# Optimization experiments

Hardware: AMD Instinct MI355X
Metric: run time of the kernel (lower is better)

## Reference

```python
import jax, jax.numpy as jnp
import numpy as np

PATCH = 16
FMAP = 14  # 224 // 16, feature-map / mask resolution
BLUR_K = np.array([[1., 2., 1.], [2., 4., 2.], [1., 2., 1.]], dtype=np.float32) / 16.0  # pascal(3), normalized


def _conv(x, w, stride, pad):
    return jax.lax.conv_general_dilated(
        x, w, (stride, stride), [(pad, pad), (pad, pad)],
        dimension_numbers=("NCHW", "OIHW", "NCHW"))


def _max_blur_pool(x):
    # MaxBlurPool2D(kernel_size=3, stride=2, max_pool_size=2, ceil_mode=False):
    x = jax.lax.reduce_window(x, -jnp.inf, jax.lax.max,
                              (1, 1, 2, 2), (1, 1, 1, 1), "VALID")
    C = x.shape[1]
    kw = jnp.broadcast_to(jnp.asarray(BLUR_K, x.dtype), (C, 1, 3, 3))
    return jax.lax.conv_general_dilated(
        x, kw, (2, 2), [(1, 1), (1, 1)],
        dimension_numbers=("NCHW", "OIHW", "NCHW"), feature_group_count=C)


def _up(m, hw):
    # upsample [B,1,FMAP,FMAP] mask to spatial size hw via repeat_interleave
    f = hw // FMAP
    return jnp.repeat(jnp.repeat(m, f, axis=2), f, axis=3)


def reference(x, masks, w1, w2):
    B = x.shape[0]
    m = masks.reshape(B, 1, FMAP, FMAP).astype(x.dtype)  # fmap-level active mask
    x = x * _up(m, x.shape[2])                 # _apply_masks: zero masked 16x16 patches
    x = _conv(x, w1, 2, 3)                     # B,64,112,112
    x = jax.nn.relu(x * _up(m, x.shape[2]))    # SparK-style sparse conv: re-mask output
    x = _max_blur_pool(x)                      # B,64,56,56
    x = _conv(x, w2, 2, 3)                     # B,768,28,28
    x = jax.nn.relu(x * _up(m, x.shape[2]))    # re-mask output of second sparse conv
    x = _max_blur_pool(x)                      # B,768,14,14
    B_, C, H, W = x.shape
    return x.reshape(B_, C, H * W).transpose(0, 2, 1)  # b (h w) c -> [B,196,768]


def setup_inputs() -> dict:
    key = jax.random.key(0)
    k1, k2, k3, k4 = jax.random.split(key, 4)
    x = jax.random.normal(k1, (64, 3, 224, 224), jnp.float32)
    masks = jax.random.randint(k2, (64, 196), 0, 2).astype(bool)
    # kaiming_normal fan_in scaling as in init_weight
    w1 = jax.random.normal(k3, (64, 3, 7, 7), jnp.float32) * np.float32(np.sqrt(2.0 / (3 * 49)))
    w2 = jax.random.normal(k4, (768, 64, 7, 7), jnp.float32) * np.float32(np.sqrt(2.0 / (64 * 49)))
    return {"x": x, "masks": masks, "w1": w1, "w2": w2}
```

## Files before the change

### kernel.cpp

```cpp
#include <hip/hip_runtime.h>
#include <stdint.h>

typedef __attribute__((ext_vector_type(8))) short short8;
typedef __attribute__((ext_vector_type(4))) float f32x4;

#define DEVFN static __device__ __forceinline__

DEVFN float bf2f(uint16_t u) { union { uint32_t i; float f; } v; v.i = ((uint32_t)u) << 16; return v.f; }
DEVFN uint16_t f2bf(float f) {
  union { float f; uint32_t i; } v; v.f = f;
  uint32_t u = v.i;
  u += 0x7fffu + ((u >> 16) & 1u);
  return (uint16_t)(u >> 16);
}
DEVFN int imin(int a, int b) { return a < b ? a : b; }

DEVFN void gl_lds16(const void* g, void* l) {
  __builtin_amdgcn_global_load_lds(
      (__attribute__((address_space(1))) void*)(void*)g,
      (__attribute__((address_space(3))) void*)l, 16, 0, 0);
}

DEVFN f32x4 mfma16(short8 a, short8 b, f32x4 c) {
  return __builtin_amdgcn_mfma_f32_16x16x32_bf16(a, b, c, 0, 0, 0);
}

static constexpr size_t OFF_XP   = 0;
static constexpr size_t OFF_W1T  = 27557888;
static constexpr size_t OFF_W2T  = 27586560;
static constexpr size_t OFF_Y1   = 32403456;
static constexpr size_t OFF_P1   = 135163904;
static constexpr size_t OFF_Y2   = 166653952;
static constexpr size_t OFF_LIST = 243724288;
static constexpr size_t OFF_CNT  = 243774464;
static constexpr size_t WS_NEED  = 243774664;

__global__ __launch_bounds__(256) void k_count(const int* __restrict__ masks, int* __restrict__ cnts) {
  int b = blockIdx.x;
  int gid = b * 256 + threadIdx.x;
  unsigned long long m = __ballot(masks[gid] != 0);
  __shared__ int wsum[4];
  if ((threadIdx.x & 63) == 0) wsum[threadIdx.x >> 6] = __popcll(m);
  __syncthreads();
  if (threadIdx.x == 0) cnts[b] = wsum[0] + wsum[1] + wsum[2] + wsum[3];
}

__global__ __launch_bounds__(256) void k_emit(const int* __restrict__ masks, const int* __restrict__ cnts,
                                              int* __restrict__ list, int* __restrict__ total) {
  int b = blockIdx.x;
  int gid = b * 256 + threadIdx.x;
  int lane = threadIdx.x & 63, wave = threadIdx.x >> 6;
  int base = 0;
  for (int i = 0; i < b; ++i) base += cnts[i];
  bool f = masks[gid] != 0;
  unsigned long long m = __ballot(f);
  __shared__ int wcnt[4];
  if (lane == 0) wcnt[wave] = __popcll(m);
  __syncthreads();
  int woff = 0;
  for (int i = 0; i < wave; ++i) woff += wcnt[i];
  if (f) list[base + woff + __popcll(m & ((1ull << lane) - 1ull))] = gid;
  if (b == 48 && threadIdx.x == 0)
    *total = base + wcnt[0] + wcnt[1] + wcnt[2] + wcnt[3];
}

__global__ __launch_bounds__(256) void k_prep(const float* __restrict__ x, const int* __restrict__ masks,
                                              uint16_t* __restrict__ xp) {
  int gid = blockIdx.x * 256 + threadIdx.x;
  int b = gid / 53824;
  int rc = gid - b * 53824;
  int r2 = rc / 232;
  int c2 = rc - r2 * 232;
  int r = r2 - 3, c = c2 - 3;
  uint16_t o0 = 0, o1 = 0, o2 = 0;
  if ((unsigned)r < 224u && (unsigned)c < 224u) {
    if (masks[b * 196 + (r >> 4) * 14 + (c >> 4)]) {
      const float* px = x + (((size_t)b * 3) * 224 + r) * 224 + c;
      o0 = f2bf(px[0]);
      o1 = f2bf(px[50176]);
      o2 = f2bf(px[100352]);
    }
  }
  ushort4 o; o.x = o0; o.y = o1; o.z = o2; o.w = 0;
  *(ushort4*)(xp + (size_t)gid * 4) = o;
}

__global__ __launch_bounds__(256) void k_wt(const float* __restrict__ w1, const float* __restrict__ w2,
                                            uint16_t* __restrict__ w1t, uint16_t* __restrict__ w2t) {
  int gid = blockIdx.x * 256 + threadIdx.x;
  if (gid < 14336) {
    int kh = gid / 2048; int r = gid - kh * 2048;
    int oc = r >> 5, slot = r & 31;
    int kw = slot >> 2, ic = slot & 3;
    float v = 0.f;
    if (kw < 7 && ic < 3) v = w1[((oc * 3 + ic) * 7 + kh) * 7 + kw];
    w1t[gid] = f2bf(v);
  } else {
    int g2 = gid - 14336;
    int khw = g2 / 49152; int r = g2 - khw * 49152;
    int oc = r >> 6, ic = r & 63;
    int kh = khw / 7, kw = khw - kh * 7;
    w2t[g2] = f2bf(w2[((oc * 64 + ic) * 7 + kh) * 7 + kw]);
  }
}

__global__ __launch_bounds__(256, 3) void k_conv1(const uint16_t* __restrict__ xp, const uint16_t* __restrict__ w1t,
                                                  const int* __restrict__ list, const int* __restrict__ count,
                                                  uint16_t* __restrict__ y1) {
  __shared__ uint16_t sB[7 * 64 * 32];
  __shared__ int sc[2];

  int cnt = *count;
  int blk = blockIdx.x;
  if (blk * 2 >= cnt) return;
  int tid = threadIdx.x, lane = tid & 63, wave = tid >> 6;
  int csw = (lane & 3) ^ ((lane >> 2) & 3);

  {
    const char* wg = (const char*)w1t;
    char* wl = (char*)sB;
#pragma unroll
    for (int t = 0; t < 7; ++t) {
      int ldsoff = t * 4096 + wave * 1024;
      int goff = t * 4096 + (wave * 16 + (lane >> 2)) * 64 + csw * 16;
      gl_lds16(wg + goff, wl + ldsoff);
    }
  }
  if (tid < 2) sc[tid] = list[imin(blk * 2 + tid, cnt - 1)];
  __syncthreads();

  int wm = wave * 32, mrow = lane & 15, kg = lane >> 4;

  const uint16_t* baseA[2];
#pragma unroll
  for (int i = 0; i < 2; ++i) {
    int row = wm + 16 * i + mrow;
    int cell = sc[row >> 6];
    int b = cell / 196, cc = cell - b * 196;
    int ci = cc / 14, cj = cc - ci * 14;
    int p = row & 63;
    int oh = ci * 8 + (p >> 3), ow = cj * 8 + (p & 7);
    baseA[i] = xp + (((size_t)(b * 232 + 2 * oh)) * 232 + 2 * ow) * 4 + kg * 8;
  }
  int ksw = (kg ^ (mrow & 3)) * 8;

  f32x4 acc[2][4];
#pragma unroll
  for (int i = 0; i < 2; ++i)
#pragma unroll
    for (int j = 0; j < 4; ++j) acc[i][j] = f32x4{0.f, 0.f, 0.f, 0.f};

#pragma unroll
  for (int kh = 0; kh < 7; ++kh) {
    short8 a0 = *(const short8*)(baseA[0] + kh * 928);
    short8 a1 = *(const short8*)(baseA[1] + kh * 928);
    const uint16_t* Bk = sB + kh * 2048;
#pragma unroll
    for (int j = 0; j < 4; ++j) {
      short8 bj = *(const short8*)(Bk + (16 * j + mrow) * 32 + ksw);
      acc[0][j] = mfma16(a0, bj, acc[0][j]);
      acc[1][j] = mfma16(a1, bj, acc[1][j]);
    }
  }

#pragma unroll
  for (int i = 0; i < 2; ++i) {
    int rbase = wm + 16 * i;
    int cellidx = blk * 2 + (rbase >> 6);
    if (cellidx >= cnt) continue;
    int cell = sc[rbase >> 6];
    int b = cell / 196, cc = cell - b * 196;
    int ci = cc / 14, cj = cc - ci * 14;
#pragma unroll
    for (int j = 0; j < 4; ++j) {
      int oc = 16 * j + mrow;
#pragma unroll
      for (int r = 0; r < 4; ++r) {
        int row = rbase + kg * 4 + r;
        int p = row & 63;
        int oh = ci * 8 + (p >> 3), ow = cj * 8 + (p & 7);
        float v = acc[i][j][r];
        v = v > 0.f ? v : 0.f;
        y1[(((size_t)(b * 112 + oh)) * 112 + ow) * 64 + oc] = f2bf(v);
      }
    }
  }
}

__global__ __launch_bounds__(256) void k_pool1(const uint16_t* __restrict__ y1, const int* __restrict__ masks,
                                               uint16_t* __restrict__ p1) {
  __shared__ uint16_t sY[18 * 18 * 64];
  int b = blockIdx.y;
  int tile = blockIdx.x;
  int tr = tile >> 3, tc = tile & 7;
  int pr0 = tr * 8, pc0 = tc * 8;
  int R0 = 2 * pr0 - 7, C0 = 2 * pc0 - 7;
  int tid = threadIdx.x;
  const int* mb = masks + b * 196;

  for (int idx = tid; idx < 2592; idx += 256) {
    int pix = idx >> 3, ch = idx & 7;
    int pr = pix / 18, pc = pix - pr * 18;
    int r = R0 + pr, c = C0 + pc;
    short8 v = {0, 0, 0, 0, 0, 0, 0, 0};
    if ((unsigned)r < 112u && (unsigned)c < 112u && mb[(r >> 3) * 14 + (c >> 3)])
      v = *(const short8*)(y1 + (((size_t)(b * 112 + r)) * 112 + c) * 64 + ch * 8);
    *(short8*)(sY + ((size_t)(pr * 18 + pc)) * 64 + ch * 8) = v;
  }
  __syncthreads();

  for (int it = tid; it < 512; it += 256) {
    int opix = it >> 3, ch = it & 7;
    int lr = opix >> 3, lc = opix & 7;
    int pr = pr0 + lr, pc = pc0 + lc;
    if (pr >= 62 || pc >= 62) continue;
    int oh = pr - 3, ow = pc - 3;
    float acc[8] = {0.f, 0.f, 0.f, 0.f, 0.f, 0.f, 0.f, 0.f};
    if ((unsigned)oh < 56u && (unsigned)ow < 56u) {
      float hm_prev[3][8];
#pragma unroll
      for (int dd = 0; dd < 4; ++dd) {
        float yv[4][8];
        const uint16_t* src = sY + ((size_t)((2 * lr + dd) * 18 + 2 * lc)) * 64 + ch * 8;
#pragma unroll
        for (int e = 0; e < 4; ++e) {
          short8 t8 = *(const short8*)(src + e * 64);
#pragma unroll
          for (int k = 0; k < 8; ++k) yv[e][k] = bf2f((uint16_t)t8[k]);
        }
        float hm[3][8];
#pragma unroll
        for (int e = 0; e < 3; ++e) {
          int qc = 2 * ow - 1 + e;
          float cv = ((unsigned)qc <= 110u) ? 1.f : 0.f;
#pragma unroll
          for (int k = 0; k < 8; ++k) hm[e][k] = cv * fmaxf(yv[e][k], yv[e + 1][k]);
        }
        if (dd > 0) {
          int d = dd - 1;
          int qr = 2 * oh - 1 + d;
          if ((unsigned)qr <= 110u) {
            float wd = (d == 1) ? 2.f : 1.f;
#pragma unroll
            for (int e = 0; e < 3; ++e) {
              float w = wd * ((e == 1) ? 2.f : 1.f);
#pragma unroll
              for (int k = 0; k < 8; ++k) acc[k] += w * fmaxf(hm_prev[e][k], hm[e][k]);
            }
          }
        }
#pragma unroll
        for (int e = 0; e < 3; ++e)
#pragma unroll
          for (int k = 0; k < 8; ++k) hm_prev[e][k] = hm[e][k];
      }
#pragma unroll
      for (int k = 0; k < 8; ++k) acc[k] *= (1.f / 16.f);
    }
    short8 o;
#pragma unroll
    for (int k = 0; k < 8; ++k) o[k] = (short)f2bf(acc[k]);
    *(short8*)(p1 + (((size_t)(b * 62 + pr)) * 62 + pc) * 64 + ch * 8) = o;
  }
}

__global__ __launch_bounds__(512, 4) void k_conv2(const uint16_t* __restrict__ p1, const uint16_t* __restrict__ w2t,
                                                  const int* __restrict__ list, const int* __restrict__ count,
                                                  uint16_t* __restrict__ y2) {
  __shared__ uint16_t sA[256 * 64];
  __shared__ uint16_t sBt[128 * 64];

  int cnt = *count;
  int gx = blockIdx.x;
  int xcd = gx & 7, s = gx >> 3;
  int y = s % 6, mtl = s / 6;
  int mt = xcd + 8 * mtl;
  if (mt * 64 >= cnt) return;
  int ocb = y * 128;
  int tid = threadIdx.x, lane = tid & 63, wave = tid >> 6;
  int csw = (lane & 7) ^ ((lane >> 3) & 7);

  int* scs = (int*)sA;
  if (tid < 64) scs[tid] = list[imin(mt * 64 + tid, cnt - 1)];
  __syncthreads();
  int qm = wave & 3, qn = wave >> 2;
  int mrow = lane & 15, kg = lane >> 4;
  int cellA[4], cellE[4];
#pragma unroll
  for (int t = 0; t < 4; ++t) cellA[t] = scs[wave * 8 + t * 2 + (lane >> 5)];
#pragma unroll
  for (int i = 0; i < 4; ++i) cellE[i] = scs[qm * 16 + 4 * i + kg];
  __syncthreads();

  const char* gA[4];
#pragma unroll
  for (int t = 0; t < 4; ++t) {
    int r = wave * 32 + t * 8 + (lane >> 3);
    int cell = cellA[t];
    int b = cell / 196, cc = cell - b * 196;
    int ci = cc / 14, cj = cc - ci * 14;
    int p = r & 3;
    int oh = 2 * ci + (p >> 1), ow = 2 * cj + (p & 1);
    gA[t] = (const char*)p1 + (((size_t)(b * 62 + 2 * oh)) * 62 + 2 * ow) * 128 + csw * 16;
  }
  const char* gB[2];
#pragma unroll
  for (int t = 0; t < 2; ++t) {
    int oc = ocb + wave * 16 + t * 8 + (lane >> 3);
    gB[t] = (const char*)w2t + (size_t)oc * 128 + csw * 16;
  }

  f32x4 acc[4][4];
#pragma unroll
  for (int i = 0; i < 4; ++i)
#pragma unroll
    for (int j = 0; j < 4; ++j) acc[i][j] = f32x4{0.f, 0.f, 0.f, 0.f};

  int sw = mrow & 7;
  int kh = 0, kw = 0;

#pragma unroll 1
  for (int it = 0; it < 49; ++it) {
    size_t offA = (size_t)(kh * 62 + kw) * 128;
    size_t offB = (size_t)it * 98304;
    char* la = (char*)sA + (wave * 32) * 128;
    char* lb = (char*)sBt + (wave * 16) * 128;
#pragma unroll
    for (int t = 0; t < 4; ++t) gl_lds16(gA[t] + offA, la + t * 1024);
#pragma unroll
    for (int t = 0; t < 2; ++t) gl_lds16(gB[t] + offB, lb + t * 1024);
    __syncthreads();
#pragma unroll
    for (int ks = 0; ks < 2; ++ks) {
      int koff = ((ks * 4 + kg) ^ sw) * 8;
      short8 a[4], bb[4];
#pragma unroll
      for (int i = 0; i < 4; ++i)
        a[i] = *(const short8*)(sA + (qm * 64 + 16 * i + mrow) * 64 + koff);
#pragma unroll
      for (int j = 0; j < 4; ++j)
        bb[j] = *(const short8*)(sBt + (qn * 64 + 16 * j + mrow) * 64 + koff);
#pragma unroll
      for (int i = 0; i < 4; ++i)
#pragma unroll
        for (int j = 0; j < 4; ++j)
          acc[i][j] = mfma16(a[i], bb[j], acc[i][j]);
    }
    __syncthreads();
    if (++kw == 7) { kw = 0; ++kh; }
  }

#pragma unroll
  for (int i = 0; i < 4; ++i) {
    int cellslot = qm * 16 + 4 * i + kg;
    int cellidx = mt * 64 + cellslot;
    if (cellidx >= cnt) continue;
    int cell = cellE[i];
    int b = cell / 196, cc = cell - b * 196;
    int ci = cc / 14, cj = cc - ci * 14;
#pragma unroll
    for (int j = 0; j < 4; ++j) {
      int oc = ocb + qn * 64 + 16 * j + mrow;
#pragma unroll
      for (int r = 0; r < 4; ++r) {
        int oh = 2 * ci + (r >> 1), ow = 2 * cj + (r & 1);
        float v = acc[i][j][r];
        v = v > 0.f ? v : 0.f;
        y2[(((size_t)(b * 784)) + oh * 28 + ow) * 768 + oc] = f2bf(v);
      }
    }
  }
}

__global__ __launch_bounds__(256) void k_pool2(const uint16_t* __restrict__ y2, const int* __restrict__ masks,
                                               float* __restrict__ out) {
  __shared__ uint16_t sY[4 * 28 * 128];
  int chunk = blockIdx.x, pi = blockIdx.y, b = blockIdx.z;
  int ch0 = chunk * 128;
  int tid = threadIdx.x;
  const int* mb = masks + b * 196;

  for (int idx = tid; idx < 1792; idx += 256) {
    int rc = idx >> 4;
    int sub = idx & 15;
    int k = rc / 28, c = rc - k * 28;
    int r = 2 * pi - 1 + k;
    short8 v = {0, 0, 0, 0, 0, 0, 0, 0};
    if ((unsigned)r < 28u && mb[(r >> 1) * 14 + (c >> 1)])
      v = *(const short8*)(y2 + (((size_t)(b * 784)) + r * 28 + c) * 768 + ch0 + sub * 8);
    *(short8*)(sY + ((size_t)(k * 28 + c)) * 128 + sub * 8) = v;
  }
  __syncthreads();

  for (int idx = tid; idx < 1792; idx += 256) {
    int pj = idx >> 7, ch = idx & 127;
    float v[4][4];
#pragma unroll
    for (int e = 0; e < 4; ++e) {
      int col = 2 * pj - 1 + e;
      bool cv = (unsigned)col < 28u;
#pragma unroll
      for (int k = 0; k < 4; ++k)
        v[k][e] = cv ? bf2f(sY[((size_t)(k * 28 + col)) * 128 + ch]) : 0.f;
    }
    float acc = 0.f;
#pragma unroll
    for (int d = 0; d < 3; ++d) {
      int q = 2 * pi - 1 + d;
      float gd = ((unsigned)q <= 26u) ? ((d == 1) ? 2.f : 1.f) : 0.f;
      float s = 0.f;
#pragma unroll
      for (int e = 0; e < 3; ++e) {
        int q2 = 2 * pj - 1 + e;
        float ge = ((unsigned)q2 <= 26u) ? ((e == 1) ? 2.f : 1.f) : 0.f;
        float m = fmaxf(fmaxf(v[d][e], v[d + 1][e]), fmaxf(v[d][e + 1], v[d + 1][e + 1]));
        s += ge * m;
      }
      acc += gd * s;
    }
    out[(((size_t)(b * 196)) + pi * 14 + pj) * 768 + ch0 + ch] = acc * (1.f / 16.f);
  }
}

extern "C" void kernel_launch(void* const* d_in, const int* in_sizes, int n_in,
                              void* d_out, int out_size, void* d_ws, size_t ws_size,
                              hipStream_t stream) {
  const float* x     = (const float*)d_in[0];
  const int*   masks = (const int*)d_in[1];
  const float* w1    = (const float*)d_in[2];
  const float* w2    = (const float*)d_in[3];

  char* ws = (char*)d_ws;
  if (ws_size < WS_NEED) return;

  uint16_t* xp  = (uint16_t*)(ws + OFF_XP);
  uint16_t* w1t = (uint16_t*)(ws + OFF_W1T);
  uint16_t* w2t = (uint16_t*)(ws + OFF_W2T);
  uint16_t* y1  = (uint16_t*)(ws + OFF_Y1);
  uint16_t* p1  = (uint16_t*)(ws + OFF_P1);
  uint16_t* y2  = (uint16_t*)(ws + OFF_Y2);
  int* list     = (int*)(ws + OFF_LIST);
  int* cnts     = (int*)(ws + OFF_CNT);
  int* total    = cnts + 49;

  k_count<<<49, 256, 0, stream>>>(masks, cnts);
  k_emit<<<49, 256, 0, stream>>>(masks, cnts, list, total);
  k_prep<<<13456, 256, 0, stream>>>(x, masks, xp);
  k_wt<<<9464, 256, 0, stream>>>(w1, w2, w1t, w2t);
  k_conv1<<<6272, 256, 0, stream>>>(xp, w1t, list, total, y1);
  k_pool1<<<dim3(64, 64), 256, 0, stream>>>(y1, masks, p1);
  k_conv2<<<1200, 512, 0, stream>>>(p1, w2t, list, total, y2);
  k_pool2<<<dim3(6, 14, 64), 256, 0, stream>>>(y2, masks, (float*)d_out);
}
```

Baseline: 395.3 us.

## Fuse conv1 with max-blur-pool per active cell and tile the w2 transpose

Conv1 and the first MaxBlurPool are merged into one kernel. Each active mask cell computes a 14x14 conv1 output region with halo into LDS, then writes its pooled 56x56-level outputs straight to p1. This drops the y1 round trip through global memory and the separate pool launch. In exchange the halo conv work is recomputed per cell, a memset of p1 is added, and the w2 weight transpose is rewritten to coalesce through LDS. Halo outputs that belong to active neighbour cells are skipped, so each p1 position is written only once.

```diff
diff --git a/kernel.cpp b/kernel.cpp
--- a/kernel.cpp
+++ b/kernel.cpp
@@ -28,7 +28,6 @@
 static constexpr size_t OFF_XP   = 0;
 static constexpr size_t OFF_W1T  = 27557888;
 static constexpr size_t OFF_W2T  = 27586560;
-static constexpr size_t OFF_Y1   = 32403456;
 static constexpr size_t OFF_P1   = 135163904;
 static constexpr size_t OFF_Y2   = 166653952;
 static constexpr size_t OFF_LIST = 243724288;
@@ -85,34 +84,51 @@
   *(ushort4*)(xp + (size_t)gid * 4) = o;
 }
 
-__global__ __launch_bounds__(256) void k_wt(const float* __restrict__ w1, const float* __restrict__ w2,
-                                            uint16_t* __restrict__ w1t, uint16_t* __restrict__ w2t) {
+__global__ __launch_bounds__(256) void k_wt1(const float* __restrict__ w1, uint16_t* __restrict__ w1t) {
   int gid = blockIdx.x * 256 + threadIdx.x;
-  if (gid < 14336) {
-    int kh = gid / 2048; int r = gid - kh * 2048;
-    int oc = r >> 5, slot = r & 31;
-    int kw = slot >> 2, ic = slot & 3;
-    float v = 0.f;
-    if (kw < 7 && ic < 3) v = w1[((oc * 3 + ic) * 7 + kh) * 7 + kw];
-    w1t[gid] = f2bf(v);
-  } else {
-    int g2 = gid - 14336;
-    int khw = g2 / 49152; int r = g2 - khw * 49152;
-    int oc = r >> 6, ic = r & 63;
-    int kh = khw / 7, kw = khw - kh * 7;
-    w2t[g2] = f2bf(w2[((oc * 64 + ic) * 7 + kh) * 7 + kw]);
-  }
-}
-
-__global__ __launch_bounds__(256, 3) void k_conv1(const uint16_t* __restrict__ xp, const uint16_t* __restrict__ w1t,
-                                                  const int* __restrict__ list, const int* __restrict__ count,
-                                                  uint16_t* __restrict__ y1) {
+  int kh = gid / 2048; int r = gid - kh * 2048;
+  int oc = r >> 5, slot = r & 31;
+  int kw = slot >> 2, ic = slot & 3;
+  float v = 0.f;
+  if (kw < 7 && ic < 3) v = w1[((oc * 3 + ic) * 7 + kh) * 7 + kw];
+  w1t[gid] = f2bf(v);
+}
+
+__global__ __launch_bounds__(256) void k_wt2(const float* __restrict__ w2, uint16_t* __restrict__ w2t) {
+  __shared__ uint16_t sw2[49 * 8 * 64];
+  int oc0 = blockIdx.x * 8;
+  int tid = threadIdx.x;
+  const float* src = w2 + (size_t)oc0 * 3136;
+  for (int idx = tid; idx < 6272; idx += 256) {
+    float4 f4 = *(const float4*)(src + idx * 4);
+    float fv[4] = {f4.x, f4.y, f4.z, f4.w};
+#pragma unroll
+    for (int k = 0; k < 4; ++k) {
+      int l = idx * 4 + k;
+      int oc = l / 3136; int rem = l - oc * 3136;
+      int ic = rem / 49;  int t = rem - ic * 49;
+      sw2[(t * 8 + oc) * 64 + ic] = f2bf(fv[k]);
+    }
+  }
+  __syncthreads();
+  for (int o = tid; o < 3136; o += 256) {
+    short8 v = *(const short8*)(sw2 + o * 8);
+    int tap = o >> 6;
+    int within = (o & 63) * 8;
+    *(short8*)(w2t + (size_t)tap * 49152 + oc0 * 64 + within) = v;
+  }
+}
+
+__global__ __launch_bounds__(256, 2) void k_c1p(const uint16_t* __restrict__ xp, const uint16_t* __restrict__ w1t,
+                                                const int* __restrict__ list, const int* __restrict__ count,
+                                                const int* __restrict__ masks, uint16_t* __restrict__ p1) {
   __shared__ uint16_t sB[7 * 64 * 32];
-  __shared__ int sc[2];
+  __shared__ uint16_t ly1[196 * 72];
+  __shared__ int sm[9];
 
   int cnt = *count;
   int blk = blockIdx.x;
-  if (blk * 2 >= cnt) return;
+  if (blk >= cnt) return;
   int tid = threadIdx.x, lane = tid & 63, wave = tid >> 6;
   int csw = (lane & 3) ^ ((lane >> 2) & 3);
 
@@ -126,141 +142,123 @@
       gl_lds16(wg + goff, wl + ldsoff);
     }
   }
-  if (tid < 2) sc[tid] = list[imin(blk * 2 + tid, cnt - 1)];
-  __syncthreads();
-
-  int wm = wave * 32, mrow = lane & 15, kg = lane >> 4;
-
-  const uint16_t* baseA[2];
-#pragma unroll
-  for (int i = 0; i < 2; ++i) {
-    int row = wm + 16 * i + mrow;
-    int cell = sc[row >> 6];
-    int b = cell / 196, cc = cell - b * 196;
-    int ci = cc / 14, cj = cc - ci * 14;
-    int p = row & 63;
-    int oh = ci * 8 + (p >> 3), ow = cj * 8 + (p & 7);
-    baseA[i] = xp + (((size_t)(b * 232 + 2 * oh)) * 232 + 2 * ow) * 4 + kg * 8;
-  }
+
+  int cell = list[blk];
+  int b = cell / 196, cc = cell - b * 196;
+  int ci = cc / 14, cj = cc - ci * 14;
+  if (tid < 9) {
+    int di = tid / 3 - 1, dj = tid % 3 - 1;
+    int ni = ci + di, nj = cj + dj;
+    sm[tid] = ((unsigned)ni < 14u && (unsigned)nj < 14u) ? masks[b * 196 + ni * 14 + nj] : 0;
+  }
+  __syncthreads();
+
+  int mrow = lane & 15, kg = lane >> 4;
   int ksw = (kg ^ (mrow & 3)) * 8;
 
-  f32x4 acc[2][4];
-#pragma unroll
-  for (int i = 0; i < 2; ++i)
+  const uint16_t* baseA[4];
+#pragma unroll
+  for (int t = 0; t < 4; ++t) {
+    int row = wave * 64 + t * 16 + mrow;
+    int pos = row < 196 ? row : 0;
+    int rl = pos / 14, cl = pos - rl * 14;
+    int oh = 8 * ci - 3 + rl, ow = 8 * cj - 3 + cl;
+    bool vld = ((unsigned)oh < 112u) && ((unsigned)ow < 112u);
+    int r0 = vld ? 2 * oh : 0;
+    int c0 = vld ? 2 * ow : 0;
+    baseA[t] = xp + (((size_t)(b * 232 + r0)) * 232 + c0) * 4 + kg * 8;
+  }
+
+  f32x4 acc[4][4];
+#pragma unroll
+  for (int i = 0; i < 4; ++i)
 #pragma unroll
     for (int j = 0; j < 4; ++j) acc[i][j] = f32x4{0.f, 0.f, 0.f, 0.f};
 
 #pragma unroll
   for (int kh = 0; kh < 7; ++kh) {
-    short8 a0 = *(const short8*)(baseA[0] + kh * 928);
-    short8 a1 = *(const short8*)(baseA[1] + kh * 928);
+    short8 a[4];
+#pragma unroll
+    for (int t = 0; t < 4; ++t) a[t] = *(const short8*)(baseA[t] + kh * 928);
     const uint16_t* Bk = sB + kh * 2048;
 #pragma unroll
     for (int j = 0; j < 4; ++j) {
       short8 bj = *(const short8*)(Bk + (16 * j + mrow) * 32 + ksw);
-      acc[0][j] = mfma16(a0, bj, acc[0][j]);
-      acc[1][j] = mfma16(a1, bj, acc[1][j]);
-    }
-  }
-
-#pragma unroll
-  for (int i = 0; i < 2; ++i) {
-    int rbase = wm + 16 * i;
-    int cellidx = blk * 2 + (rbase >> 6);
-    if (cellidx >= cnt) continue;
-    int cell = sc[rbase >> 6];
-    int b = cell / 196, cc = cell - b * 196;
-    int ci = cc / 14, cj = cc - ci * 14;
-#pragma unroll
-    for (int j = 0; j < 4; ++j) {
-      int oc = 16 * j + mrow;
-#pragma unroll
-      for (int r = 0; r < 4; ++r) {
-        int row = rbase + kg * 4 + r;
-        int p = row & 63;
-        int oh = ci * 8 + (p >> 3), ow = cj * 8 + (p & 7);
-        float v = acc[i][j][r];
-        v = v > 0.f ? v : 0.f;
-        y1[(((size_t)(b * 112 + oh)) * 112 + ow) * 64 + oc] = f2bf(v);
+#pragma unroll
+      for (int t = 0; t < 4; ++t) acc[t][j] = mfma16(a[t], bj, acc[t][j]);
+    }
+  }
+
+#pragma unroll
+  for (int t = 0; t < 4; ++t) {
+#pragma unroll
+    for (int r = 0; r < 4; ++r) {
+      int row = wave * 64 + t * 16 + kg * 4 + r;
+      if (row >= 196) continue;
+      int rl = row / 14, cl = row - rl * 14;
+      int oh = 8 * ci - 3 + rl, ow = 8 * cj - 3 + cl;
+      int dI = (rl < 3) ? 0 : ((rl < 11) ? 1 : 2);
+      int dJ = (cl < 3) ? 0 : ((cl < 11) ? 1 : 2);
+      bool act = ((unsigned)oh < 112u) && ((unsigned)ow < 112u) && (sm[dI * 3 + dJ] != 0);
+#pragma unroll
+      for (int j = 0; j < 4; ++j) {
+        int oc = 16 * j + mrow;
+        float v = acc[t][j][r];
+        v = act ? (v > 0.f ? v : 0.f) : 0.f;
+        ly1[row * 72 + oc] = f2bf(v);
       }
     }
   }
-}
-
-__global__ __launch_bounds__(256) void k_pool1(const uint16_t* __restrict__ y1, const int* __restrict__ masks,
-                                               uint16_t* __restrict__ p1) {
-  __shared__ uint16_t sY[18 * 18 * 64];
-  int b = blockIdx.y;
-  int tile = blockIdx.x;
-  int tr = tile >> 3, tc = tile & 7;
-  int pr0 = tr * 8, pc0 = tc * 8;
-  int R0 = 2 * pr0 - 7, C0 = 2 * pc0 - 7;
-  int tid = threadIdx.x;
-  const int* mb = masks + b * 196;
-
-  for (int idx = tid; idx < 2592; idx += 256) {
-    int pix = idx >> 3, ch = idx & 7;
-    int pr = pix / 18, pc = pix - pr * 18;
-    int r = R0 + pr, c = C0 + pc;
-    short8 v = {0, 0, 0, 0, 0, 0, 0, 0};
-    if ((unsigned)r < 112u && (unsigned)c < 112u && mb[(r >> 3) * 14 + (c >> 3)])
-      v = *(const short8*)(y1 + (((size_t)(b * 112 + r)) * 112 + c) * 64 + ch * 8);
-    *(short8*)(sY + ((size_t)(pr * 18 + pc)) * 64 + ch * 8) = v;
-  }
-  __syncthreads();
-
-  for (int it = tid; it < 512; it += 256) {
-    int opix = it >> 3, ch = it & 7;
-    int lr = opix >> 3, lc = opix & 7;
-    int pr = pr0 + lr, pc = pc0 + lc;
-    if (pr >= 62 || pc >= 62) continue;
-    int oh = pr - 3, ow = pc - 3;
-    float acc[8] = {0.f, 0.f, 0.f, 0.f, 0.f, 0.f, 0.f, 0.f};
-    if ((unsigned)oh < 56u && (unsigned)ow < 56u) {
-      float hm_prev[3][8];
-#pragma unroll
-      for (int dd = 0; dd < 4; ++dd) {
-        float yv[4][8];
-        const uint16_t* src = sY + ((size_t)((2 * lr + dd) * 18 + 2 * lc)) * 64 + ch * 8;
-#pragma unroll
-        for (int e = 0; e < 4; ++e) {
-          short8 t8 = *(const short8*)(src + e * 64);
-#pragma unroll
-          for (int k = 0; k < 8; ++k) yv[e][k] = bf2f((uint16_t)t8[k]);
+  __syncthreads();
+
+  for (int idx = tid; idx < 576; idx += 256) {
+    int epos = idx >> 4;
+    int chw = (idx & 15) * 4;
+    int er = epos / 6 - 1, ec = epos % 6 - 1;
+    int oh = 4 * ci + er, ow = 4 * cj + ec;
+    if ((unsigned)oh >= 56u || (unsigned)ow >= 56u) continue;
+    bool center = ((unsigned)er < 4u) && ((unsigned)ec < 4u);
+    if (!center) {
+      int dIo = (er < 0) ? 0 : ((er > 3) ? 2 : 1);
+      int dJo = (ec < 0) ? 0 : ((ec > 3) ? 2 : 1);
+      if (sm[dIo * 3 + dJo] != 0) continue;
+    }
+    float v[4][4][4];
+#pragma unroll
+    for (int rr = 0; rr < 4; ++rr) {
+      int rl = 2 * er + 2 + rr;
+#pragma unroll
+      for (int ccx = 0; ccx < 4; ++ccx) {
+        int cl = 2 * ec + 2 + ccx;
+        ushort4 t4 = *(const ushort4*)(ly1 + (rl * 14 + cl) * 72 + chw);
+        v[rr][ccx][0] = bf2f(t4.x); v[rr][ccx][1] = bf2f(t4.y);
+        v[rr][ccx][2] = bf2f(t4.z); v[rr][ccx][3] = bf2f(t4.w);
+      }
+    }
+    float o[4] = {0.f, 0.f, 0.f, 0.f};
+#pragma unroll
+    for (int d = 0; d < 3; ++d) {
+      int q = 2 * oh - 1 + d;
+      float gd = ((unsigned)q <= 110u) ? ((d == 1) ? 2.f : 1.f) : 0.f;
+#pragma unroll
+      for (int e = 0; e < 3; ++e) {
+        int q2 = 2 * ow - 1 + e;
+        float ge = ((unsigned)q2 <= 110u) ? ((e == 1) ? 2.f : 1.f) : 0.f;
+        float w = gd * ge;
+#pragma unroll
+        for (int u = 0; u < 4; ++u) {
+          float m = fmaxf(fmaxf(v[d][e][u], v[d][e + 1][u]),
+                          fmaxf(v[d + 1][e][u], v[d + 1][e + 1][u]));
+          o[u] += w * m;
         }
-        float hm[3][8];
-#pragma unroll
-        for (int e = 0; e < 3; ++e) {
-          int qc = 2 * ow - 1 + e;
-          float cv = ((unsigned)qc <= 110u) ? 1.f : 0.f;
-#pragma unroll
-          for (int k = 0; k < 8; ++k) hm[e][k] = cv * fmaxf(yv[e][k], yv[e + 1][k]);
-        }
-        if (dd > 0) {
-          int d = dd - 1;
-          int qr = 2 * oh - 1 + d;
-          if ((unsigned)qr <= 110u) {
-            float wd = (d == 1) ? 2.f : 1.f;
-#pragma unroll
-            for (int e = 0; e < 3; ++e) {
-              float w = wd * ((e == 1) ? 2.f : 1.f);
-#pragma unroll
-              for (int k = 0; k < 8; ++k) acc[k] += w * fmaxf(hm_prev[e][k], hm[e][k]);
-            }
-          }
-        }
-#pragma unroll
-        for (int e = 0; e < 3; ++e)
-#pragma unroll
-          for (int k = 0; k < 8; ++k) hm_prev[e][k] = hm[e][k];
       }
-#pragma unroll
-      for (int k = 0; k < 8; ++k) acc[k] *= (1.f / 16.f);
-    }
-    short8 o;
-#pragma unroll
-    for (int k = 0; k < 8; ++k) o[k] = (short)f2bf(acc[k]);
-    *(short8*)(p1 + (((size_t)(b * 62 + pr)) * 62 + pc) * 64 + ch * 8) = o;
+    }
+    ushort4 ov;
+    ov.x = f2bf(o[0] * (1.f / 16.f));
+    ov.y = f2bf(o[1] * (1.f / 16.f));
+    ov.z = f2bf(o[2] * (1.f / 16.f));
+    ov.w = f2bf(o[3] * (1.f / 16.f));
+    *(ushort4*)(p1 + (((size_t)(b * 62 + (oh + 3))) * 62 + (ow + 3)) * 64 + chw) = ov;
   }
 }
 
@@ -436,19 +434,19 @@
   uint16_t* xp  = (uint16_t*)(ws + OFF_XP);
   uint16_t* w1t = (uint16_t*)(ws + OFF_W1T);
   uint16_t* w2t = (uint16_t*)(ws + OFF_W2T);
-  uint16_t* y1  = (uint16_t*)(ws + OFF_Y1);
   uint16_t* p1  = (uint16_t*)(ws + OFF_P1);
   uint16_t* y2  = (uint16_t*)(ws + OFF_Y2);
   int* list     = (int*)(ws + OFF_LIST);
   int* cnts     = (int*)(ws + OFF_CNT);
   int* total    = cnts + 49;
 
+  hipMemsetAsync(p1, 0, 31490048, stream);
   k_count<<<49, 256, 0, stream>>>(masks, cnts);
   k_emit<<<49, 256, 0, stream>>>(masks, cnts, list, total);
   k_prep<<<13456, 256, 0, stream>>>(x, masks, xp);
-  k_wt<<<9464, 256, 0, stream>>>(w1, w2, w1t, w2t);
-  k_conv1<<<6272, 256, 0, stream>>>(xp, w1t, list, total, y1);
-  k_pool1<<<dim3(64, 64), 256, 0, stream>>>(y1, masks, p1);
+  k_wt1<<<56, 256, 0, stream>>>(w1, w1t);
+  k_wt2<<<96, 256, 0, stream>>>(w2, w2t);
+  k_c1p<<<12544, 256, 0, stream>>>(xp, w1t, list, total, masks, p1);
   k_conv2<<<1200, 512, 0, stream>>>(p1, w2t, list, total, y2);
   k_pool2<<<dim3(6, 14, 64), 256, 0, stream>>>(y2, masks, (float*)d_out);
 }
```

New measurement: 430.7 us. +8.9%, slower.
